# Kernel optimization log

Measured on AMD Instinct MI355X. Metric: run time of the kernel, lower is better.

The kernel has to match this reference:

```python
import jax, jax.numpy as jnp
import numpy as np

B, H, N, D = 8, 8, 1024, 64

def setup_inputs() -> dict:
    key = jax.random.key(0)
    k = jax.random.split(key, 7)
    Q = jax.random.normal(k[0], (B, H, N, D), dtype=jnp.float32)
    K = jax.random.normal(k[1], (B, H, N, D), dtype=jnp.float32)
    V = jax.random.normal(k[2], (B, H, N, D), dtype=jnp.float32)
    attention_mask = jax.random.randint(k[3], (B, 1, N, N), 0, 2).astype(bool)
    adjacency_matrix = jax.random.randint(k[4], (B, N, N), 0, 2).astype(jnp.float32)
    row_subtracted_distance_matrix = jax.random.normal(k[5], (B, N, N), dtype=jnp.float32)
    weight_A = jax.random.normal(k[6], (1, H, 1, 1), dtype=jnp.float32)
    return {
        'Q': Q, 'K': K, 'V': V,
        'attention_mask': attention_mask,
        'adjacency_matrix': adjacency_matrix,
        'row_subtracted_distance_matrix': row_subtracted_distance_matrix,
        'weight_A': weight_A,
    }


def reference(Q, K, V, attention_mask, adjacency_matrix,
              row_subtracted_distance_matrix, weight_A):
    # Note: due to an __init__ bug in the source, the A_Geo branch is dead
    # (self.use_A_Geo is overwritten with None), and row_subtracted_distance_matrix
    # is validated but never used in the math. dropout p=0.0 is identity.
    scale = Q.shape[-1] ** 0.5
    # [B,H,N,N] raw scores
    s = jnp.einsum('bhnd,bhmd->bhnm', Q, K)
    # mask_attention_score(attn, M, 0.0): masked positions set to 0.0 pre-softmax
    s = jnp.where(attention_mask, s, jnp.float32(0.0))
    # adjacency bias: B_A = s * (A * weight_A); s = s + B_A
    A = adjacency_matrix[:, None]          # [B,1,N,N]
    s = s * (1.0 + A * weight_A)           # fused s + s*(A*w_A)
    s = s / jnp.float32(scale)
    attn_weight = jax.nn.softmax(s, axis=-1)
    out = jnp.einsum('bhnm,bhmd->bhnd', attn_weight, V)
    return (out, attn_weight)
```

## Files before the change

### kernel.cpp

```cpp
#include <hip/hip_runtime.h>


typedef __attribute__((ext_vector_type(8))) short short8;
typedef __attribute__((ext_vector_type(4))) short short4v;
typedef __attribute__((ext_vector_type(4))) float float4v;

#define BDIM 8
#define HDIM 8
#define NDIM 1024
#define DDIM 64

__device__ __forceinline__ short f2bf(float x){
  unsigned int u = __float_as_uint(x);
  unsigned int r = (u + 0x7fffu + ((u >> 16) & 1u)) >> 16;
  return (short)r;
}
__device__ __forceinline__ float bf2f(short s){
  return __uint_as_float(((unsigned int)(unsigned short)s) << 16);
}
__device__ __forceinline__ int swz(int r, int c){
  return r * 64 + ((((c >> 3) ^ (r & 7))) << 3) + (c & 7);
}
__device__ __forceinline__ short8 ldsFrag(const short* base, int row, int ch){
  return *(const short8*)(base + row * 64 + ((ch ^ (row & 7)) << 3));
}
__device__ __forceinline__ float4v mfma16(short8 a, short8 b, float4v c){
  return __builtin_amdgcn_mfma_f32_16x16x32_bf16(a, b, c, 0, 0, 0);
}

__device__ __forceinline__ void stageHL(const float* __restrict__ gsrc,
                                        short* ldsH, short* ldsL, int tid){
  const int r  = tid >> 2;
  const int cb = (tid & 3) << 2;
  #pragma unroll
  for (int k = 0; k < 4; ++k){
    const int c = cb + (k << 4);
    float4v v = *(const float4v*)(gsrc + r * 64 + c);
    short4v hv, lv;
    #pragma unroll
    for (int j = 0; j < 4; ++j){
      float x = v[j];
      short hb = f2bf(x);
      hv[j] = hb;
      lv[j] = f2bf(x - bf2f(hb));
    }
    const int idx = swz(r, c);
    *(short4v*)(ldsH + idx) = hv;
    *(short4v*)(ldsL + idx) = lv;
  }
}

__device__ __forceinline__ void stageVT(const float* __restrict__ gsrc,
                                        short* ldsH, short* ldsL, int tid){
  const int m  = tid >> 2;
  const int db = (tid & 3) << 2;
  #pragma unroll
  for (int k = 0; k < 4; ++k){
    const int d0 = db + (k << 4);
    float4v v = *(const float4v*)(gsrc + m * 64 + d0);
    #pragma unroll
    for (int j = 0; j < 4; ++j){
      float x = v[j];
      short hb = f2bf(x);
      const int idx = swz(d0 + j, m);
      ldsH[idx] = hb;
      ldsL[idx] = f2bf(x - bf2f(hb));
    }
  }
}

__global__ void detect_kernel(const unsigned int* __restrict__ m, int* __restrict__ flag){
  __shared__ unsigned int fl;
  if (threadIdx.x == 0) fl = 0u;
  __syncthreads();
  unsigned int loc = 0u;
  #pragma unroll
  for (int j = 0; j < 4; ++j){
    unsigned int w = m[threadIdx.x * 4 + j];
    if (w == 0x3f800000u) loc |= 2u;
    else if (w > 1u)      loc |= 1u;
  }
  atomicOr(&fl, loc);
  __syncthreads();
  if (threadIdx.x == 0){
    int code = 0;
    if (fl & 2u) code = 2;
    else if (fl & 1u) code = 1;
    flag[0] = code;
  }
}

__global__ void pack_kernel(const void* __restrict__ maskp, const float* __restrict__ adjp,
                            const int* __restrict__ flagp, unsigned int* __restrict__ pk){
  const int wi = blockIdx.x * 256 + threadIdx.x;
  const size_t e0 = (size_t)wi << 4;
  const int fl = flagp[0];
  unsigned int word = 0u;
  if (fl == 0){
    const int* mp = (const int*)maskp + e0;
    #pragma unroll
    for (int j = 0; j < 16; ++j) if (mp[j] != 0) word |= (1u << (2 * j));
  } else if (fl == 1){
    const unsigned char* mp = (const unsigned char*)maskp + e0;
    #pragma unroll
    for (int j = 0; j < 16; ++j) if (mp[j] != 0) word |= (1u << (2 * j));
  } else {
    const float* mp = (const float*)maskp + e0;
    #pragma unroll
    for (int j = 0; j < 16; ++j) if (mp[j] != 0.f) word |= (1u << (2 * j));
  }
  const float* ap = adjp + e0;
  #pragma unroll
  for (int j = 0; j < 16; ++j) if (ap[j] != 0.f) word |= (2u << (2 * j));
  pk[wi] = word;
}

template<int PACKED>
__global__ __launch_bounds__(256) void msrsa_main(
    const float* __restrict__ Q, const float* __restrict__ K, const float* __restrict__ V,
    const void* __restrict__ maskp, const float* __restrict__ adjp,
    const float* __restrict__ wAp,
    float* __restrict__ outp, float* __restrict__ attnp,
    const unsigned int* __restrict__ pk, const int* __restrict__ flagp)
{
  const int p   = blockIdx.x;
  const int blk = (p & 7) * 128 + (p >> 3);
  const int b  = blk >> 7;
  const int h  = (blk >> 4) & 7;
  const int rb = blk & 15;
  const int n0 = rb << 6;
  const int tid  = threadIdx.x;
  const int wid  = tid >> 6;
  const int lane = tid & 63;
  const int g    = lane >> 4;
  const int q    = lane & 15;

  const size_t bh = (size_t)(b * HDIM + h);
  const float* Qb = Q + bh * (NDIM * DDIM) + (size_t)n0 * DDIM;
  const float* Kb = K + bh * (NDIM * DDIM);
  const float* Vb = V + bh * (NDIM * DDIM);
  const float c0 = 0.125f;
  const float cA = (1.0f + wAp[h]) * 0.125f;
  int flag = 0;
  if (!PACKED) flag = flagp[0];
  const size_t bNN = (size_t)b * ((size_t)NDIM * NDIM);

  __shared__ __align__(16) short A0h[4096], A0l[4096];
  __shared__ __align__(16) short A1h[4096], A1l[4096];
  __shared__ __align__(16) short A2h[4096], A2l[4096];

  stageHL(Qb, A0h, A0l, tid);
  __syncthreads();
  const int arow = (wid << 4) + q;
  short8 qh[2], ql[2];
  qh[0] = ldsFrag(A0h, arow, g);  qh[1] = ldsFrag(A0h, arow, g + 4);
  ql[0] = ldsFrag(A0l, arow, g);  ql[1] = ldsFrag(A0l, arow, g + 4);

  int nloc[4];
  #pragma unroll
  for (int i = 0; i < 4; ++i) nloc[i] = (wid << 4) + (g << 2) + i;

  float psum[4] = {0.f, 0.f, 0.f, 0.f};
  for (int ms = 0; ms < 16; ++ms){
    const int m0 = ms << 6;
    __syncthreads();
    stageHL(Kb + m0 * DDIM, A1h, A1l, tid);
    __syncthreads();
    #pragma unroll
    for (int mt = 0; mt < 4; ++mt){
      float4v acc = {0.f, 0.f, 0.f, 0.f};
      const int brow = (mt << 4) + q;
      #pragma unroll
      for (int ks = 0; ks < 2; ++ks){
        short8 kh = ldsFrag(A1h, brow, g + (ks << 2));
        short8 kl = ldsFrag(A1l, brow, g + (ks << 2));
        acc = mfma16(qh[ks], kh, acc);
        acc = mfma16(qh[ks], kl, acc);
        acc = mfma16(ql[ks], kh, acc);
      }
      #pragma unroll
      for (int i = 0; i < 4; ++i){
        const int n = n0 + nloc[i];
        float coef;
        if (PACKED){
          unsigned int wv = pk[((unsigned)b << 16) + ((unsigned)n << 6) + (unsigned)((m0 >> 4) + mt)];
          unsigned int bits = (wv >> (q << 1)) & 3u;
          coef = (bits & 1u) ? ((bits & 2u) ? cA : c0) : 0.0f;
        } else {
          const size_t ei = bNN + (size_t)n * NDIM + (size_t)(m0 + (mt << 4) + q);
          bool mk;
          if (flag == 0)      mk = ((const int*)maskp)[ei] != 0;
          else if (flag == 1) mk = ((const unsigned char*)maskp)[ei] != 0;
          else                mk = ((const float*)maskp)[ei] != 0.f;
          float av = adjp[ei];
          coef = mk ? ((av != 0.f) ? cA : c0) : 0.f;
        }
        psum[i] += __expf(acc[i] * coef);
      }
    }
  }
  float inv[4];
  #pragma unroll
  for (int i = 0; i < 4; ++i){
    float s = psum[i];
    s += __shfl_xor(s, 1, 16);
    s += __shfl_xor(s, 2, 16);
    s += __shfl_xor(s, 4, 16);
    s += __shfl_xor(s, 8, 16);
    inv[i] = 1.0f / s;
  }

  float4v oacc[4];
  #pragma unroll
  for (int dt = 0; dt < 4; ++dt) oacc[dt] = (float4v){0.f, 0.f, 0.f, 0.f};

  float* aRow[4];
  #pragma unroll
  for (int i = 0; i < 4; ++i)
    aRow[i] = attnp + (bh * NDIM + (size_t)(n0 + nloc[i])) * (size_t)NDIM;

  for (int ms = 0; ms < 16; ++ms){
    const int m0 = ms << 6;
    __syncthreads();
    stageHL(Kb + m0 * DDIM, A1h, A1l, tid);
    stageVT(Vb + m0 * DDIM, A2h, A2l, tid);
    __syncthreads();
    #pragma unroll
    for (int mt = 0; mt < 4; ++mt){
      float4v acc = {0.f, 0.f, 0.f, 0.f};
      const int brow = (mt << 4) + q;
      #pragma unroll
      for (int ks = 0; ks < 2; ++ks){
        short8 kh = ldsFrag(A1h, brow, g + (ks << 2));
        short8 kl = ldsFrag(A1l, brow, g + (ks << 2));
        acc = mfma16(qh[ks], kh, acc);
        acc = mfma16(qh[ks], kl, acc);
        acc = mfma16(ql[ks], kh, acc);
      }
      #pragma unroll
      for (int i = 0; i < 4; ++i){
        const int n = n0 + nloc[i];
        float coef;
        if (PACKED){
          unsigned int wv = pk[((unsigned)b << 16) + ((unsigned)n << 6) + (unsigned)((m0 >> 4) + mt)];
          unsigned int bits = (wv >> (q << 1)) & 3u;
          coef = (bits & 1u) ? ((bits & 2u) ? cA : c0) : 0.0f;
        } else {
          const size_t ei = bNN + (size_t)n * NDIM + (size_t)(m0 + (mt << 4) + q);
          bool mk;
          if (flag == 0)      mk = ((const int*)maskp)[ei] != 0;
          else if (flag == 1) mk = ((const unsigned char*)maskp)[ei] != 0;
          else                mk = ((const float*)maskp)[ei] != 0.f;
          float av = adjp[ei];
          coef = mk ? ((av != 0.f) ? cA : c0) : 0.f;
        }
        float p2 = __expf(acc[i] * coef);
        float at = p2 * inv[i];
        aRow[i][m0 + (mt << 4) + q] = at;
        short ph = f2bf(at);
        const int pi = swz(nloc[i], (mt << 4) + q);
        A0h[pi] = ph;
        A0l[pi] = f2bf(at - bf2f(ph));
      }
    }
    __syncthreads();
    #pragma unroll
    for (int ks = 0; ks < 2; ++ks){
      short8 pah = ldsFrag(A0h, arow, g + (ks << 2));
      short8 pal = ldsFrag(A0l, arow, g + (ks << 2));
      #pragma unroll
      for (int dt = 0; dt < 4; ++dt){
        short8 vh = ldsFrag(A2h, (dt << 4) + q, g + (ks << 2));
        short8 vl = ldsFrag(A2l, (dt << 4) + q, g + (ks << 2));
        oacc[dt] = mfma16(pah, vh, oacc[dt]);
        oacc[dt] = mfma16(pah, vl, oacc[dt]);
        oacc[dt] = mfma16(pal, vh, oacc[dt]);
      }
    }
  }

  #pragma unroll
  for (int dt = 0; dt < 4; ++dt){
    #pragma unroll
    for (int i = 0; i < 4; ++i){
      outp[(bh * NDIM + (size_t)(n0 + nloc[i])) * DDIM + (dt << 4) + q] = oacc[dt][i];
    }
  }
}

extern "C" void kernel_launch(void* const* d_in, const int* in_sizes, int n_in,
                              void* d_out, int out_size, void* d_ws, size_t ws_size,
                              hipStream_t stream){
  const float* Q    = (const float*)d_in[0];
  const float* K    = (const float*)d_in[1];
  const float* V    = (const float*)d_in[2];
  const void*  mskp = d_in[3];
  const float* adjp = (const float*)d_in[4];
  const float* wAp  = (const float*)d_in[6];

  float* outp  = (float*)d_out;
  float* attnp = outp + (size_t)BDIM * HDIM * NDIM * DDIM;

  int* flagp = (int*)d_ws;
  unsigned int* pkbuf = (unsigned int*)((char*)d_ws + 256);
  const bool packed = ws_size >= ((size_t)2 * 1024 * 1024 + 256);

  hipLaunchKernelGGL(detect_kernel, dim3(1), dim3(256), 0, stream,
                     (const unsigned int*)mskp, flagp);
  if (packed){
    hipLaunchKernelGGL(pack_kernel, dim3(2048), dim3(256), 0, stream,
                       mskp, adjp, flagp, pkbuf);
    hipLaunchKernelGGL(msrsa_main<1>, dim3(1024), dim3(256), 0, stream,
                       Q, K, V, mskp, adjp, wAp, outp, attnp, pkbuf, flagp);
  } else {
    hipLaunchKernelGGL(msrsa_main<0>, dim3(1024), dim3(256), 0, stream,
                       Q, K, V, mskp, adjp, wAp, outp, attnp, pkbuf, flagp);
  }
}
```

Baseline: 567.4 us.

## Precompute bf16 hi/lo swizzled Q/K/V tiles and load them via direct global-to-LDS copies

Adds a precvt kernel that splits Q, K and V into bf16 high/low pairs once, writing them in the swizzled LDS layout (V transposed) into a 48MB workspace buffer. The main kernel then fills its LDS tiles with global_load_lds 16-byte copies instead of converting fp32 on every tile stage. This removes the conversion work that was repeated across the 16 row blocks per head and across both passes. The pack kernel is also rewritten to use coalesced vector loads through an LDS transpose. The cost is an extra kernel launch and extra workspace traffic, and the new path only runs when the workspace is large enough.

```diff
diff --git a/kernel.cpp b/kernel.cpp
--- a/kernel.cpp
+++ b/kernel.cpp
@@ -4,6 +4,7 @@
 typedef __attribute__((ext_vector_type(8))) short short8;
 typedef __attribute__((ext_vector_type(4))) short short4v;
 typedef __attribute__((ext_vector_type(4))) float float4v;
+typedef __attribute__((ext_vector_type(4))) unsigned int uint4v;
 
 #define BDIM 8
 #define HDIM 8
@@ -26,6 +27,19 @@
 }
 __device__ __forceinline__ float4v mfma16(short8 a, short8 b, float4v c){
   return __builtin_amdgcn_mfma_f32_16x16x32_bf16(a, b, c, 0, 0, 0);
+}
+
+__device__ __forceinline__ void gload16(const void* g, void* l){
+  __builtin_amdgcn_global_load_lds(
+      (const __attribute__((address_space(1))) unsigned int*)g,
+      (__attribute__((address_space(3))) unsigned int*)l, 16, 0, 0);
+}
+__device__ __forceinline__ void copyTile(const char* g, char* l, int wid, int lane){
+  #pragma unroll
+  for (int c = 0; c < 4; ++c){
+    gload16(g + (c << 12) + (wid << 10) + (lane << 4),
+            l + (c << 12) + (wid << 10));
+  }
 }
 
 __device__ __forceinline__ void stageHL(const float* __restrict__ gsrc,
@@ -49,7 +63,6 @@
     *(short4v*)(ldsL + idx) = lv;
   }
 }
-
 __device__ __forceinline__ void stageVT(const float* __restrict__ gsrc,
                                         short* ldsH, short* ldsL, int tid){
   const int m  = tid >> 2;
@@ -90,38 +103,129 @@
   }
 }
 
-__global__ void pack_kernel(const void* __restrict__ maskp, const float* __restrict__ adjp,
-                            const int* __restrict__ flagp, unsigned int* __restrict__ pk){
-  const int wi = blockIdx.x * 256 + threadIdx.x;
-  const size_t e0 = (size_t)wi << 4;
+__global__ __launch_bounds__(256) void pack_kernel(const void* __restrict__ maskp,
+                                                   const float* __restrict__ adjp,
+                                                   const int* __restrict__ flagp,
+                                                   unsigned int* __restrict__ pk){
+  __shared__ unsigned int st[256 * 17];
+  const int t = threadIdx.x;
+  const size_t ebase = (size_t)blockIdx.x * 4096;
   const int fl = flagp[0];
   unsigned int word = 0u;
-  if (fl == 0){
-    const int* mp = (const int*)maskp + e0;
-    #pragma unroll
-    for (int j = 0; j < 16; ++j) if (mp[j] != 0) word |= (1u << (2 * j));
-  } else if (fl == 1){
-    const unsigned char* mp = (const unsigned char*)maskp + e0;
-    #pragma unroll
-    for (int j = 0; j < 16; ++j) if (mp[j] != 0) word |= (1u << (2 * j));
+
+  if (fl == 1){
+    uint4v mv = *(const uint4v*)((const unsigned char*)maskp + ebase + (size_t)t * 16);
+    #pragma unroll
+    for (int j = 0; j < 16; ++j){
+      unsigned int byte = (mv[j >> 2] >> ((j & 3) * 8)) & 0xffu;
+      if (byte) word |= (1u << (2 * j));
+    }
   } else {
-    const float* mp = (const float*)maskp + e0;
-    #pragma unroll
-    for (int j = 0; j < 16; ++j) if (mp[j] != 0.f) word |= (1u << (2 * j));
-  }
-  const float* ap = adjp + e0;
-  #pragma unroll
-  for (int j = 0; j < 16; ++j) if (ap[j] != 0.f) word |= (2u << (2 * j));
-  pk[wi] = word;
-}
-
-template<int PACKED>
+    const unsigned int* mp = (const unsigned int*)maskp + ebase;
+    #pragma unroll
+    for (int p = 0; p < 4; ++p){
+      uint4v v = *(const uint4v*)(mp + (size_t)((p << 8) + t) * 4);
+      #pragma unroll
+      for (int j = 0; j < 4; ++j){
+        const int E = ((p << 8) + t) * 4 + j;
+        st[(E >> 4) * 17 + (E & 15)] = v[j];
+      }
+    }
+    __syncthreads();
+    if (fl == 0){
+      #pragma unroll
+      for (int j = 0; j < 16; ++j) if (st[t * 17 + j] != 0u) word |= (1u << (2 * j));
+    } else {
+      #pragma unroll
+      for (int j = 0; j < 16; ++j) if ((st[t * 17 + j] << 1) != 0u) word |= (1u << (2 * j));
+    }
+    __syncthreads();
+  }
+
+  {
+    const unsigned int* ap = (const unsigned int*)adjp + ebase;
+    #pragma unroll
+    for (int p = 0; p < 4; ++p){
+      uint4v v = *(const uint4v*)(ap + (size_t)((p << 8) + t) * 4);
+      #pragma unroll
+      for (int j = 0; j < 4; ++j){
+        const int E = ((p << 8) + t) * 4 + j;
+        st[(E >> 4) * 17 + (E & 15)] = v[j];
+      }
+    }
+    __syncthreads();
+    #pragma unroll
+    for (int j = 0; j < 16; ++j) if ((st[t * 17 + j] << 1) != 0u) word |= (2u << (2 * j));
+  }
+  pk[(size_t)blockIdx.x * 256 + t] = word;
+}
+
+__global__ __launch_bounds__(256) void precvt_kernel(const float* __restrict__ Q,
+                                                     const float* __restrict__ K,
+                                                     const float* __restrict__ V,
+                                                     char* __restrict__ cvt){
+  __shared__ float lt[64][65];
+  const int job = blockIdx.x;
+  const int arr = job >> 10;
+  const int pt  = job & 1023;
+  const float* srcBase = (arr == 0) ? Q : ((arr == 1) ? K : V);
+  const float* src = srcBase + ((size_t)(pt >> 4) * NDIM + (size_t)(pt & 15) * 64) * DDIM;
+  char* dst = cvt + ((size_t)job << 14);
+  short* dh = (short*)dst;
+  short* dl = (short*)(dst + 8192);
+  const int t = threadIdx.x;
+
+  if (arr < 2){
+    const int r = t >> 2;
+    #pragma unroll
+    for (int k = 0; k < 2; ++k){
+      const int cc = ((t & 3) << 1) + k;
+      const int cs = cc ^ (r & 7);
+      float4v v0 = *(const float4v*)(src + r * 64 + cs * 8);
+      float4v v1 = *(const float4v*)(src + r * 64 + cs * 8 + 4);
+      short8 hv, lv;
+      #pragma unroll
+      for (int j = 0; j < 4; ++j){
+        short hb = f2bf(v0[j]); hv[j] = hb;     lv[j] = f2bf(v0[j] - bf2f(hb));
+        short h2 = f2bf(v1[j]); hv[j + 4] = h2; lv[j + 4] = f2bf(v1[j] - bf2f(h2));
+      }
+      *(short8*)(dh + r * 64 + cc * 8) = hv;
+      *(short8*)(dl + r * 64 + cc * 8) = lv;
+    }
+  } else {
+    const int m = t >> 2;
+    #pragma unroll
+    for (int k = 0; k < 4; ++k){
+      const int c = ((t & 3) << 2) + (k << 4);
+      float4v v = *(const float4v*)(src + m * 64 + c);
+      lt[m][c] = v[0]; lt[m][c + 1] = v[1]; lt[m][c + 2] = v[2]; lt[m][c + 3] = v[3];
+    }
+    __syncthreads();
+    const int d = t >> 2;
+    #pragma unroll
+    for (int k = 0; k < 2; ++k){
+      const int cc = ((t & 3) << 1) + k;
+      const int ms = (cc ^ (d & 7)) << 3;
+      short8 hv, lv;
+      #pragma unroll
+      for (int j = 0; j < 8; ++j){
+        float x = lt[ms + j][d];
+        short hb = f2bf(x); hv[j] = hb; lv[j] = f2bf(x - bf2f(hb));
+      }
+      *(short8*)(dh + d * 64 + cc * 8) = hv;
+      *(short8*)(dl + d * 64 + cc * 8) = lv;
+    }
+  }
+}
+
+template<int MODE>
 __global__ __launch_bounds__(256) void msrsa_main(
     const float* __restrict__ Q, const float* __restrict__ K, const float* __restrict__ V,
     const void* __restrict__ maskp, const float* __restrict__ adjp,
     const float* __restrict__ wAp,
     float* __restrict__ outp, float* __restrict__ attnp,
-    const unsigned int* __restrict__ pk, const int* __restrict__ flagp)
+    const unsigned int* __restrict__ pk, const int* __restrict__ flagp,
+    const char* __restrict__ cvt)
 {
   const int p   = blockIdx.x;
   const int blk = (p & 7) * 128 + (p >> 3);
@@ -139,17 +243,24 @@
   const float* Qb = Q + bh * (NDIM * DDIM) + (size_t)n0 * DDIM;
   const float* Kb = K + bh * (NDIM * DDIM);
   const float* Vb = V + bh * (NDIM * DDIM);
+  const char* Qc = cvt + (((size_t)0 + bh * 16 + rb) << 14);
+  const char* Kc = cvt + (((size_t)1024 + bh * 16) << 14);
+  const char* Vc = cvt + (((size_t)2048 + bh * 16) << 14);
   const float c0 = 0.125f;
   const float cA = (1.0f + wAp[h]) * 0.125f;
   int flag = 0;
-  if (!PACKED) flag = flagp[0];
+  if (MODE == 0) flag = flagp[0];
   const size_t bNN = (size_t)b * ((size_t)NDIM * NDIM);
 
-  __shared__ __align__(16) short A0h[4096], A0l[4096];
-  __shared__ __align__(16) short A1h[4096], A1l[4096];
-  __shared__ __align__(16) short A2h[4096], A2l[4096];
-
-  stageHL(Qb, A0h, A0l, tid);
+  __shared__ __align__(16) char A0[16384];
+  __shared__ __align__(16) char A1[16384];
+  __shared__ __align__(16) char A2[16384];
+  short* A0h = (short*)A0;  short* A0l = (short*)(A0 + 8192);
+  short* A1h = (short*)A1;  short* A1l = (short*)(A1 + 8192);
+  short* A2h = (short*)A2;  short* A2l = (short*)(A2 + 8192);
+
+  if (MODE == 2) copyTile(Qc, A0, wid, lane);
+  else           stageHL(Qb, A0h, A0l, tid);
   __syncthreads();
   const int arow = (wid << 4) + q;
   short8 qh[2], ql[2];
@@ -164,7 +275,8 @@
   for (int ms = 0; ms < 16; ++ms){
     const int m0 = ms << 6;
     __syncthreads();
-    stageHL(Kb + m0 * DDIM, A1h, A1l, tid);
+    if (MODE == 2) copyTile(Kc + ((size_t)ms << 14), A1, wid, lane);
+    else           stageHL(Kb + m0 * DDIM, A1h, A1l, tid);
     __syncthreads();
     #pragma unroll
     for (int mt = 0; mt < 4; ++mt){
@@ -182,7 +294,7 @@
       for (int i = 0; i < 4; ++i){
         const int n = n0 + nloc[i];
         float coef;
-        if (PACKED){
+        if (MODE >= 1){
           unsigned int wv = pk[((unsigned)b << 16) + ((unsigned)n << 6) + (unsigned)((m0 >> 4) + mt)];
           unsigned int bits = (wv >> (q << 1)) & 3u;
           coef = (bits & 1u) ? ((bits & 2u) ? cA : c0) : 0.0f;
@@ -222,8 +334,13 @@
   for (int ms = 0; ms < 16; ++ms){
     const int m0 = ms << 6;
     __syncthreads();
-    stageHL(Kb + m0 * DDIM, A1h, A1l, tid);
-    stageVT(Vb + m0 * DDIM, A2h, A2l, tid);
+    if (MODE == 2){
+      copyTile(Kc + ((size_t)ms << 14), A1, wid, lane);
+      copyTile(Vc + ((size_t)ms << 14), A2, wid, lane);
+    } else {
+      stageHL(Kb + m0 * DDIM, A1h, A1l, tid);
+      stageVT(Vb + m0 * DDIM, A2h, A2l, tid);
+    }
     __syncthreads();
     #pragma unroll
     for (int mt = 0; mt < 4; ++mt){
@@ -241,7 +358,7 @@
       for (int i = 0; i < 4; ++i){
         const int n = n0 + nloc[i];
         float coef;
-        if (PACKED){
+        if (MODE >= 1){
           unsigned int wv = pk[((unsigned)b << 16) + ((unsigned)n << 6) + (unsigned)((m0 >> 4) + mt)];
           unsigned int bits = (wv >> (q << 1)) & 3u;
           coef = (bits & 1u) ? ((bits & 2u) ? cA : c0) : 0.0f;
@@ -303,17 +420,26 @@
 
   int* flagp = (int*)d_ws;
   unsigned int* pkbuf = (unsigned int*)((char*)d_ws + 256);
-  const bool packed = ws_size >= ((size_t)2 * 1024 * 1024 + 256);
+  char* cvtbuf = (char*)d_ws + 256 + (size_t)2 * 1024 * 1024;
+  const size_t needPk  = 256 + (size_t)2 * 1024 * 1024;
+  const size_t needCvt = needPk + (size_t)48 * 1024 * 1024;
 
   hipLaunchKernelGGL(detect_kernel, dim3(1), dim3(256), 0, stream,
                      (const unsigned int*)mskp, flagp);
-  if (packed){
+  if (ws_size >= needCvt){
+    hipLaunchKernelGGL(pack_kernel, dim3(2048), dim3(256), 0, stream,
+                       mskp, adjp, flagp, pkbuf);
+    hipLaunchKernelGGL(precvt_kernel, dim3(3072), dim3(256), 0, stream,
+                       Q, K, V, cvtbuf);
+    hipLaunchKernelGGL(msrsa_main<2>, dim3(1024), dim3(256), 0, stream,
+                       Q, K, V, mskp, adjp, wAp, outp, attnp, pkbuf, flagp, cvtbuf);
+  } else if (ws_size >= needPk){
     hipLaunchKernelGGL(pack_kernel, dim3(2048), dim3(256), 0, stream,
                        mskp, adjp, flagp, pkbuf);
     hipLaunchKernelGGL(msrsa_main<1>, dim3(1024), dim3(256), 0, stream,
-                       Q, K, V, mskp, adjp, wAp, outp, attnp, pkbuf, flagp);
+                       Q, K, V, mskp, adjp, wAp, outp, attnp, pkbuf, flagp, cvtbuf);
   } else {
     hipLaunchKernelGGL(msrsa_main<0>, dim3(1024), dim3(256), 0, stream,
-                       Q, K, V, mskp, adjp, wAp, outp, attnp, pkbuf, flagp);
-  }
-}
+                       Q, K, V, mskp, adjp, wAp, outp, attnp, pkbuf, flagp, cvtbuf);
+  }
+}
```

New measurement: 508.0 us. -10.5%, faster.
